# Optimization experiments

Measured on AMD Instinct MI355X. Metric: run time of the kernel, lower is better.

The kernel has to match this reference:

```python
import jax, jax.numpy as jnp
import numpy as np
import math

B, N, DIM, H, D = 2, 2048, 1024, 16, 64
EXPECTED_K = 1.0
LAYERSCALE_INIT = 0.001
EPS = 1e-6  # flax LayerNorm default


def layer_norm(x, scale, bias):
    mu = jnp.mean(x, axis=-1, keepdims=True)
    var = jnp.mean((x - mu) ** 2, axis=-1, keepdims=True)
    return (x - mu) * jax.lax.rsqrt(var + EPS) * scale + bias


def setup_inputs() -> dict:
    key = jax.random.key(0)
    ks = jax.random.split(key, 8)
    s = DIM ** -0.5
    x = jax.random.normal(ks[0], (B, N, DIM), jnp.float32)
    Wq = jax.random.normal(ks[1], (DIM, H * D), jnp.float32) * s
    Wk = jax.random.normal(ks[2], (DIM, H * D), jnp.float32) * s
    Wv = jax.random.normal(ks[3], (DIM, H * D), jnp.float32) * s
    Wo = jax.random.normal(ks[4], (H * D, DIM), jnp.float32) * ((H * D) ** -0.5)
    e = EXPECTED_K / N
    init_bias = jnp.full((1, 1, 1, 1), math.log(e / (1.0 - e)), jnp.float32)
    return {
        'x': x,
        'Wq': Wq, 'bq': jnp.zeros((H * D,), jnp.float32),
        'Wk': Wk, 'bk': jnp.zeros((H * D,), jnp.float32),
        'Wv': Wv, 'bv': jnp.zeros((H * D,), jnp.float32),
        'qn_scale': jnp.ones((D,), jnp.float32), 'qn_bias': jnp.zeros((D,), jnp.float32),
        'kn_scale': jnp.ones((D,), jnp.float32), 'kn_bias': jnp.zeros((D,), jnp.float32),
        'init_bias': init_bias,
        'Wo': Wo, 'bo': jnp.zeros((DIM,), jnp.float32),
        'gamma': jnp.full((DIM,), LAYERSCALE_INIT, jnp.float32),
    }


def reference(x, Wq, bq, Wk, bk, Wv, bv, qn_scale, qn_bias, kn_scale, kn_bias,
              init_bias, Wo, bo, gamma):
    Bv, Nv, _ = x.shape
    q = (x @ Wq + bq).reshape(Bv, Nv, H, D)
    k = (x @ Wk + bk).reshape(Bv, Nv, H, D)
    v = (x @ Wv + bv).reshape(Bv, Nv, H, D)
    q = layer_norm(q, qn_scale, qn_bias)
    k = layer_norm(k, kn_scale, kn_bias)
    q = jnp.swapaxes(q, 1, 2)  # [B,H,N,D]
    k = jnp.swapaxes(k, 1, 2)
    v = jnp.swapaxes(v, 1, 2)
    # NOTE: original code computes scale = head_dim**-0.5 but never applies it.
    attn_logits = jnp.einsum('bhid,bhjd->bhij', q, k)
    attn_weights = jax.nn.sigmoid(attn_logits + init_bias)
    out = jnp.einsum('bhij,bhjd->bhid', attn_weights, v)
    out = jnp.swapaxes(out, 1, 2).reshape(Bv, Nv, H * D)
    out = out @ Wo + bo
    return out * gamma
```

## Files before the change

kernel.cpp:

```cpp
#include <hip/hip_runtime.h>

#define DEV static __device__ __forceinline__

typedef __bf16 bf16x8 __attribute__((ext_vector_type(8)));
typedef __bf16 bf16x4 __attribute__((ext_vector_type(4)));
typedef float f32x4 __attribute__((ext_vector_type(4)));
typedef float f32x16 __attribute__((ext_vector_type(16)));
typedef unsigned int uint4v __attribute__((ext_vector_type(4)));
typedef unsigned short ushort4v __attribute__((ext_vector_type(4)));
using u16 = unsigned short;

#define NN 2048
#define DIMD 1024

DEV u16 f2bf(float f) {
    __bf16 b = (__bf16)f;
    return __builtin_bit_cast(u16, b);
}
DEV float bf2f(u16 s) {
    unsigned u = ((unsigned)s) << 16;
    return __builtin_bit_cast(float, u);
}
DEV bf16x8 load16(const u16* p) { return __builtin_bit_cast(bf16x8, *(const uint4v*)p); }
DEV f32x4 mfma16(bf16x8 a, bf16x8 b, f32x4 c) {
    return __builtin_amdgcn_mfma_f32_16x16x32_bf16(a, b, c, 0, 0, 0);
}
DEV f32x16 mfma32(bf16x8 a, bf16x8 b, f32x16 c) {
    return __builtin_amdgcn_mfma_f32_32x32x16_bf16(a, b, c, 0, 0, 0);
}
DEV void gl_lds16(const u16* g, u16* l) {
    __builtin_amdgcn_global_load_lds((const __attribute__((address_space(1))) void*)g,
                                     (__attribute__((address_space(3))) void*)l, 16, 0, 0);
}


__global__ __launch_bounds__(256) void k_prep(const float* __restrict__ x,
                                              const float* __restrict__ s0,
                                              const float* __restrict__ s1,
                                              const float* __restrict__ s2,
                                              const float* __restrict__ s3,
                                              u16* __restrict__ xb,
                                              u16* __restrict__ wqkv_t,
                                              u16* __restrict__ wo_t) {
    __shared__ float tile[32][33];
    const int z = blockIdx.z;
    if (z < 4) {
        const float* src = (z == 0) ? s0 : (z == 1) ? s1 : (z == 2) ? s2 : s3;
        u16* dst = (z < 3) ? (wqkv_t + (size_t)z * 1024 * 1024) : wo_t;
        int tx = threadIdx.x & 31, ty = threadIdx.x >> 5;
        int kb = blockIdx.y * 32, nb = blockIdx.x * 32;
#pragma unroll
        for (int j = 0; j < 4; ++j)
            tile[ty + 8 * j][tx] = src[(size_t)(kb + ty + 8 * j) * 1024 + nb + tx];
        __syncthreads();
#pragma unroll
        for (int j = 0; j < 4; ++j)
            dst[(size_t)(nb + ty + 8 * j) * 1024 + kb + tx] = f2bf(tile[tx][ty + 8 * j]);
    } else {
        const int bidx = blockIdx.y * 32 + blockIdx.x;
#pragma unroll
        for (int q = 0; q < 4; ++q) {
            int i = bidx * 1024 + q * 256 + threadIdx.x;
            float4 v = ((const float4*)x)[i];
            ushort4v o;
            o[0] = f2bf(v.x); o[1] = f2bf(v.y); o[2] = f2bf(v.z); o[3] = f2bf(v.w);
            *(ushort4v*)(xb + (size_t)i * 4) = o;
        }
    }
}

__global__ __launch_bounds__(256) void k_gemm_qkv(const u16* __restrict__ A,
                                                  const u16* __restrict__ Bt,
                                                  const float* __restrict__ bq,
                                                  const float* __restrict__ bk,
                                                  const float* __restrict__ bv,
                                                  const float* __restrict__ qs,
                                                  const float* __restrict__ qb,
                                                  const float* __restrict__ ks,
                                                  const float* __restrict__ kb_,
                                                  u16* __restrict__ Qf,
                                                  u16* __restrict__ Kf,
                                                  u16* __restrict__ Vf) {
    __shared__ u16 lds[4][2][64 * 32 * 2];
    const int K = 1024;
    const int m0 = blockIdx.x * 128, n0 = blockIdx.y * 128;
    const int tid = threadIdx.x;
    const int lane = tid & 63, w = tid >> 6;
    const int wr = w >> 1, wc = w & 1;
    const int li = lane & 15, g = lane >> 4;
    const int l7 = li & 7;

    f32x4 acc[4][4] = {};

    u16* lA = &lds[w][0][0];
    u16* lB = &lds[w][1][0];
    const int lr = lane >> 3;
    const int lc = (lane & 7) ^ lr;
    const u16* gA = A + (size_t)(m0 + wr * 64 + lr) * K + lc * 8;
    const u16* gB = Bt + (size_t)(n0 + wc * 64 + lr) * K + lc * 8;

    auto STAGE = [&](int k0) {
#pragma unroll
        for (int i = 0; i < 8; ++i) {
            gl_lds16(gA + (size_t)(i * 8) * K + k0, lA + i * 512);
            gl_lds16(gB + (size_t)(i * 8) * K + k0, lB + i * 512);
        }
    };

    STAGE(0);
    asm volatile("s_waitcnt vmcnt(0)" ::: "memory");

    for (int t = 0; t < 16; ++t) {
        bf16x8 af[4][2], bfv[4][2];
#pragma unroll
        for (int mi = 0; mi < 4; ++mi) {
            const int row = mi * 16 + li;
#pragma unroll
            for (int s = 0; s < 2; ++s)
                af[mi][s] = load16(&lA[row * 64 + (((s * 4 + g) ^ l7) * 8)]);
        }
#pragma unroll
        for (int ni = 0; ni < 4; ++ni) {
            const int row = ni * 16 + li;
#pragma unroll
            for (int s = 0; s < 2; ++s)
                bfv[ni][s] = load16(&lB[row * 64 + (((s * 4 + g) ^ l7) * 8)]);
        }
        asm volatile("s_waitcnt lgkmcnt(0)" ::: "memory");
        __builtin_amdgcn_sched_barrier(0);
        if (t < 15) STAGE((t + 1) * 64);
#pragma unroll
        for (int mi = 0; mi < 4; ++mi)
#pragma unroll
            for (int ni = 0; ni < 4; ++ni) {
                acc[mi][ni] = mfma16(af[mi][0], bfv[ni][0], acc[mi][ni]);
                acc[mi][ni] = mfma16(af[mi][1], bfv[ni][1], acc[mi][ni]);
            }
        asm volatile("s_waitcnt vmcnt(0)" ::: "memory");
    }

    const int col0 = n0 + wc * 64;
    const int seg = col0 >> 10;
    const int hcol = col0 & 1023;
    const int h = hcol >> 6;

    if (seg < 2) {
        const float* S = (seg == 0) ? qs : ks;
        const float* Bb = (seg == 0) ? qb : kb_;
        const float* bias = (seg == 0) ? bq : bk;
        u16* dst = (seg == 0) ? Qf : Kf;
        const float sc = (seg == 0) ? -1.44269504f : 1.0f;
        float lnS[4], lnB[4], bv4[4];
#pragma unroll
        for (int ni = 0; ni < 4; ++ni) {
            int d = ni * 16 + li;
            lnS[ni] = S[d] * sc; lnB[ni] = Bb[d] * sc; bv4[ni] = bias[hcol + d];
        }
#pragma unroll
        for (int mi = 0; mi < 4; ++mi) {
#pragma unroll
            for (int r = 0; r < 4; ++r) {
                float v0 = acc[mi][0][r] + bv4[0];
                float v1 = acc[mi][1][r] + bv4[1];
                float v2 = acc[mi][2][r] + bv4[2];
                float v3 = acc[mi][3][r] + bv4[3];
                float s1 = v0 + v1 + v2 + v3;
                float s2 = v0 * v0 + v1 * v1 + v2 * v2 + v3 * v3;
#pragma unroll
                for (int o = 1; o < 16; o <<= 1) {
                    s1 += __shfl_xor(s1, o);
                    s2 += __shfl_xor(s2, o);
                }
                float mu = s1 * (1.0f / 64.0f);
                float var = s2 * (1.0f / 64.0f) - mu * mu;
                float rsv = rsqrtf(var + 1e-6f);
                int row = m0 + wr * 64 + mi * 16 + 4 * g + r;
                int bseq = row >> 11, n = row & 2047;
                size_t base = ((size_t)(bseq * 16 + h)) * 131072 +
                              ((size_t)(n >> 5) * 4) * 512 + (size_t)(n & 31) * 8 +
                              (li >> 3) * 256 + (li & 7);
                dst[base + 0 * 512] = f2bf((v0 - mu) * rsv * lnS[0] + lnB[0]);
                dst[base + 1 * 512] = f2bf((v1 - mu) * rsv * lnS[1] + lnB[1]);
                dst[base + 2 * 512] = f2bf((v2 - mu) * rsv * lnS[2] + lnB[2]);
                dst[base + 3 * 512] = f2bf((v3 - mu) * rsv * lnS[3] + lnB[3]);
            }
        }
    } else {
        float bv4[4];
#pragma unroll
        for (int ni = 0; ni < 4; ++ni) bv4[ni] = bv[hcol + ni * 16 + li];
#pragma unroll
        for (int mi = 0; mi < 4; ++mi) {
#pragma unroll
            for (int r = 0; r < 4; ++r) {
                int row = m0 + wr * 64 + mi * 16 + 4 * g + r;
                int bseq = row >> 11, j = row & 2047;
                size_t vb_ = ((size_t)(bseq * 16 + h)) * 131072 +
                             ((size_t)((j >> 5) * 4 + ((j >> 4) & 1))) * 512 +
                             (size_t)(((j >> 3) & 1) * 32) * 8 + (j & 7);
#pragma unroll
                for (int ni = 0; ni < 4; ++ni)
                    Vf[vb_ + (ni >> 1) * 1024 + ((ni & 1) * 16 + li) * 8] =
                        f2bf(acc[mi][ni][r] + bv4[ni]);
            }
        }
    }
}

__global__ __launch_bounds__(256) void k_gemm_out(const u16* __restrict__ A,
                                                  const u16* __restrict__ Bt,
                                                  const float* __restrict__ bias,
                                                  const float* __restrict__ gamma,
                                                  float* __restrict__ out) {
    __shared__ u16 lds[4][2][64 * 32 * 2];
    const int K = 1024, ldc = 1024;
    const int m0 = blockIdx.x * 128, n0 = blockIdx.y * 128;
    const int tid = threadIdx.x;
    const int lane = tid & 63, w = tid >> 6;
    const int wr = w >> 1, wc = w & 1;
    const int li = lane & 15, g = lane >> 4;
    const int l7 = li & 7;

    f32x4 acc[4][4] = {};

    u16* lA = &lds[w][0][0];
    u16* lB = &lds[w][1][0];
    const int lr = lane >> 3;
    const int lc = (lane & 7) ^ lr;
    const u16* gA = A + (size_t)(m0 + wr * 64 + lr) * K + lc * 8;
    const u16* gB = Bt + (size_t)(n0 + wc * 64 + lr) * K + lc * 8;

    auto STAGE = [&](int k0) {
#pragma unroll
        for (int i = 0; i < 8; ++i) {
            gl_lds16(gA + (size_t)(i * 8) * K + k0, lA + i * 512);
            gl_lds16(gB + (size_t)(i * 8) * K + k0, lB + i * 512);
        }
    };

    STAGE(0);
    asm volatile("s_waitcnt vmcnt(0)" ::: "memory");

    for (int t = 0; t < 16; ++t) {
        bf16x8 af[4][2], bfv[4][2];
#pragma unroll
        for (int mi = 0; mi < 4; ++mi) {
            const int row = mi * 16 + li;
#pragma unroll
            for (int s = 0; s < 2; ++s)
                af[mi][s] = load16(&lA[row * 64 + (((s * 4 + g) ^ l7) * 8)]);
        }
#pragma unroll
        for (int ni = 0; ni < 4; ++ni) {
            const int row = ni * 16 + li;
#pragma unroll
            for (int s = 0; s < 2; ++s)
                bfv[ni][s] = load16(&lB[row * 64 + (((s * 4 + g) ^ l7) * 8)]);
        }
        asm volatile("s_waitcnt lgkmcnt(0)" ::: "memory");
        __builtin_amdgcn_sched_barrier(0);
        if (t < 15) STAGE((t + 1) * 64);
#pragma unroll
        for (int mi = 0; mi < 4; ++mi)
#pragma unroll
            for (int ni = 0; ni < 4; ++ni) {
                acc[mi][ni] = mfma16(af[mi][0], bfv[ni][0], acc[mi][ni]);
                acc[mi][ni] = mfma16(af[mi][1], bfv[ni][1], acc[mi][ni]);
            }
        asm volatile("s_waitcnt vmcnt(0)" ::: "memory");
    }

#pragma unroll
    for (int mi = 0; mi < 4; ++mi) {
        int row = m0 + wr * 64 + mi * 16 + 4 * g;
#pragma unroll
        for (int ni = 0; ni < 4; ++ni) {
            int col = n0 + wc * 64 + ni * 16 + li;
            float bv_ = bias[col], gv = gamma[col];
            f32x4 v = acc[mi][ni];
#pragma unroll
            for (int r = 0; r < 4; ++r)
                out[(size_t)(row + r) * ldc + col] = (v[r] + bv_) * gv;
        }
    }
}

__global__ __launch_bounds__(256, 2) void k_attn(const u16* __restrict__ Qf,
                                                 const u16* __restrict__ Kf,
                                                 const u16* __restrict__ Vf,
                                                 const float* __restrict__ ib,
                                                 u16* __restrict__ attn_out) {
    __shared__ float red[2][64][65];
    const int bid = blockIdx.x;
    const int xcd = bid & 7, idx = bid >> 3;
    const int bh = xcd * 4 + (idx >> 5);
    const int iblk = idx & 31;
    const int b = bh >> 4, h = bh & 15;
    const int tid = threadIdx.x;
    const int jq = tid >> 6, lane = tid & 63;
    const int l32 = lane & 31, hi = lane >> 5;
    const float c0 = -ib[0] * 1.44269504f;
    const u16* Qb = Qf + (size_t)bh * 131072;
    const u16* Kb = Kf + (size_t)bh * 131072;
    const u16* Vb = Vf + (size_t)bh * 131072;
    const int it0 = iblk * 2;

    bf16x8 qf[2][4];
#pragma unroll
    for (int t = 0; t < 2; ++t)
#pragma unroll
        for (int s = 0; s < 4; ++s)
            qf[t][s] = load16(Qb + ((size_t)((it0 + t) * 4 + s)) * 512 + lane * 8);

    f32x16 accO[2][2] = {};
    const u16* kb0 = Kb + (size_t)(jq * 16) * 2048;
    const u16* vb0 = Vb + (size_t)(jq * 16) * 2048;

    f32x16 cinit;
#pragma unroll
    for (int r = 0; r < 16; ++r) cinit[r] = c0;

    bf16x8 kf[2][4], vf[2][2][2];
#pragma unroll
    for (int s = 0; s < 4; ++s) kf[0][s] = load16(kb0 + s * 512 + lane * 8);
#pragma unroll
    for (int s = 0; s < 4; ++s) kf[1][s] = load16(kb0 + 2048 + s * 512 + lane * 8);
#pragma unroll
    for (int db = 0; db < 2; ++db)
#pragma unroll
        for (int js = 0; js < 2; ++js)
            vf[0][db][js] = load16(vb0 + (db * 2 + js) * 512 + lane * 8);
    f32x16 sa0 = cinit, sa1;
#pragma unroll
    for (int s = 0; s < 4; ++s) sa0 = mfma32(kf[0][s], qf[0][s], sa0);

#pragma unroll 2
    for (int jt = 0; jt < 16; ++jt) {
        const int cur = jt & 1, nxt = cur ^ 1;
        if (jt < 15) {
            const u16* vbn = vb0 + (size_t)(jt + 1) * 2048;
#pragma unroll
            for (int db = 0; db < 2; ++db)
#pragma unroll
                for (int js = 0; js < 2; ++js)
                    vf[nxt][db][js] = load16(vbn + (db * 2 + js) * 512 + lane * 8);
        }
        __builtin_amdgcn_s_setprio(1);
        sa1 = cinit;
#pragma unroll
        for (int s = 0; s < 4; ++s) sa1 = mfma32(kf[cur][s], qf[1][s], sa1);
        __builtin_amdgcn_s_setprio(0);
        if (jt < 14) {
            const u16* kbn = kb0 + (size_t)(jt + 2) * 2048;
#pragma unroll
            for (int s = 0; s < 4; ++s) kf[cur][s] = load16(kbn + s * 512 + lane * 8);
        }
        bf16x8 p00, p01;
        {
            float p[16];
#pragma unroll
            for (int r = 0; r < 16; ++r) {
                float e = __builtin_amdgcn_exp2f(sa0[r]);
                p[r] = __builtin_amdgcn_rcpf(1.0f + e);
            }
            unsigned wd[8];
#pragma unroll
            for (int u2 = 0; u2 < 8; ++u2) {
                unsigned r_;
                asm("v_cvt_pk_bf16_f32 %0, %1, %2"
                    : "=v"(r_) : "v"(p[2 * u2]), "v"(p[2 * u2 + 1]));
                wd[u2] = r_;
            }
            asm("v_permlane32_swap_b32 %0, %1" : "+v"(wd[0]), "+v"(wd[2]));
            asm("v_permlane32_swap_b32 %0, %1" : "+v"(wd[1]), "+v"(wd[3]));
            asm("v_permlane32_swap_b32 %0, %1" : "+v"(wd[4]), "+v"(wd[6]));
            asm("v_permlane32_swap_b32 %0, %1" : "+v"(wd[5]), "+v"(wd[7]));
            uint4v u0 = {wd[0], wd[1], wd[2], wd[3]};
            uint4v u1 = {wd[4], wd[5], wd[6], wd[7]};
            p00 = __builtin_bit_cast(bf16x8, u0);
            p01 = __builtin_bit_cast(bf16x8, u1);
        }
        __builtin_amdgcn_s_setprio(1);
        accO[0][0] = mfma32(vf[cur][0][0], p00, accO[0][0]);
        accO[0][0] = mfma32(vf[cur][0][1], p01, accO[0][0]);
        accO[0][1] = mfma32(vf[cur][1][0], p00, accO[0][1]);
        accO[0][1] = mfma32(vf[cur][1][1], p01, accO[0][1]);
        if (jt < 15) {
            sa0 = cinit;
#pragma unroll
            for (int s = 0; s < 4; ++s) sa0 = mfma32(kf[nxt][s], qf[0][s], sa0);
        }
        __builtin_amdgcn_s_setprio(0);
        bf16x8 p10, p11;
        {
            float p[16];
#pragma unroll
            for (int r = 0; r < 16; ++r) {
                float e = __builtin_amdgcn_exp2f(sa1[r]);
                p[r] = __builtin_amdgcn_rcpf(1.0f + e);
            }
            unsigned wd[8];
#pragma unroll
            for (int u2 = 0; u2 < 8; ++u2) {
                unsigned r_;
                asm("v_cvt_pk_bf16_f32 %0, %1, %2"
                    : "=v"(r_) : "v"(p[2 * u2]), "v"(p[2 * u2 + 1]));
                wd[u2] = r_;
            }
            asm("v_permlane32_swap_b32 %0, %1" : "+v"(wd[0]), "+v"(wd[2]));
            asm("v_permlane32_swap_b32 %0, %1" : "+v"(wd[1]), "+v"(wd[3]));
            asm("v_permlane32_swap_b32 %0, %1" : "+v"(wd[4]), "+v"(wd[6]));
            asm("v_permlane32_swap_b32 %0, %1" : "+v"(wd[5]), "+v"(wd[7]));
            uint4v u0 = {wd[0], wd[1], wd[2], wd[3]};
            uint4v u1 = {wd[4], wd[5], wd[6], wd[7]};
            p10 = __builtin_bit_cast(bf16x8, u0);
            p11 = __builtin_bit_cast(bf16x8, u1);
        }
        __builtin_amdgcn_s_setprio(1);
        accO[1][0] = mfma32(vf[cur][0][0], p10, accO[1][0]);
        accO[1][0] = mfma32(vf[cur][0][1], p11, accO[1][0]);
        accO[1][1] = mfma32(vf[cur][1][0], p10, accO[1][1]);
        accO[1][1] = mfma32(vf[cur][1][1], p11, accO[1][1]);
        __builtin_amdgcn_s_setprio(0);
    }

    if (jq & 1) {
#pragma unroll
        for (int t = 0; t < 2; ++t)
#pragma unroll
            for (int db = 0; db < 2; ++db)
#pragma unroll
                for (int r = 0; r < 16; ++r)
                    red[jq >> 1][t * 32 + l32][db * 32 + (r & 3) + 8 * (r >> 2) + 4 * hi] =
                        accO[t][db][r];
    }
    __syncthreads();
    if (!(jq & 1)) {
#pragma unroll
        for (int t = 0; t < 2; ++t)
#pragma unroll
            for (int db = 0; db < 2; ++db)
#pragma unroll
                for (int r = 0; r < 16; ++r)
                    accO[t][db][r] +=
                        red[jq >> 1][t * 32 + l32][db * 32 + (r & 3) + 8 * (r >> 2) + 4 * hi];
    }
    __syncthreads();
    if (jq == 2) {
#pragma unroll
        for (int t = 0; t < 2; ++t)
#pragma unroll
            for (int db = 0; db < 2; ++db)
#pragma unroll
                for (int r = 0; r < 16; ++r)
                    red[0][t * 32 + l32][db * 32 + (r & 3) + 8 * (r >> 2) + 4 * hi] =
                        accO[t][db][r];
    }
    __syncthreads();
    if (jq == 0) {
#pragma unroll
        for (int t = 0; t < 2; ++t)
#pragma unroll
            for (int db = 0; db < 2; ++db)
#pragma unroll
                for (int r = 0; r < 16; ++r)
                    accO[t][db][r] +=
                        red[0][t * 32 + l32][db * 32 + (r & 3) + 8 * (r >> 2) + 4 * hi];
#pragma unroll
        for (int t = 0; t < 2; ++t) {
            const int i = it0 * 32 + t * 32 + l32;
#pragma unroll
            for (int db = 0; db < 2; ++db)
#pragma unroll
                for (int q = 0; q < 4; ++q) {
                    int d = db * 32 + 8 * q + 4 * hi;
                    bf16x4 o4;
#pragma unroll
                    for (int r = 0; r < 4; ++r) o4[r] = (__bf16)accO[t][db][4 * q + r];
                    *(bf16x4*)&attn_out[(size_t)(b * NN + i) * 1024 + h * 64 + d] = o4;
                }
        }
    }
}


extern "C" void kernel_launch(void* const* d_in, const int* in_sizes, int n_in,
                              void* d_out, int out_size, void* d_ws, size_t ws_size,
                              hipStream_t stream) {
    (void)in_sizes; (void)n_in; (void)out_size; (void)ws_size;
    const float* x     = (const float*)d_in[0];
    const float* Wq    = (const float*)d_in[1];
    const float* bq    = (const float*)d_in[2];
    const float* Wk    = (const float*)d_in[3];
    const float* bk    = (const float*)d_in[4];
    const float* Wv    = (const float*)d_in[5];
    const float* bv    = (const float*)d_in[6];
    const float* qn_s  = (const float*)d_in[7];
    const float* qn_b  = (const float*)d_in[8];
    const float* kn_s  = (const float*)d_in[9];
    const float* kn_b  = (const float*)d_in[10];
    const float* ib    = (const float*)d_in[11];
    const float* Wo    = (const float*)d_in[12];
    const float* bo    = (const float*)d_in[13];
    const float* gamma = (const float*)d_in[14];
    float* out = (float*)d_out;

    char* ws = (char*)d_ws;
    size_t off = 0;
    auto alloc = [&](size_t bytes) -> void* {
        void* p = ws + off;
        off += (bytes + 255) & ~(size_t)255;
        return p;
    };
    u16* xb       = (u16*)alloc((size_t)4096 * 1024 * 2);
    u16* wqkv_t   = (u16*)alloc((size_t)3072 * 1024 * 2);
    u16* wo_t     = (u16*)alloc((size_t)1024 * 1024 * 2);
    u16* Qf       = (u16*)alloc((size_t)32 * 131072 * 2);
    u16* Kf       = (u16*)alloc((size_t)32 * 131072 * 2);
    u16* Vf       = (u16*)alloc((size_t)32 * 131072 * 2);
    u16* attn_out = (u16*)alloc((size_t)4096 * 1024 * 2);

    k_prep<<<dim3(32, 32, 5), 256, 0, stream>>>(x, Wq, Wk, Wv, Wo, xb, wqkv_t, wo_t);
    k_gemm_qkv<<<dim3(32, 24), 256, 0, stream>>>(xb, wqkv_t, bq, bk, bv,
                                                 qn_s, qn_b, kn_s, kn_b, Qf, Kf, Vf);
    k_attn<<<1024, 256, 0, stream>>>(Qf, Kf, Vf, ib, attn_out);
    k_gemm_out<<<dim3(32, 8), 256, 0, stream>>>(attn_out, wo_t, bo, gamma, out);
}
```

Before: 116.5 us.

## Use 256x256 shared-LDS tiles with double-buffered prefetch in QKV GEMM

Rewrites the QKV projection GEMM to use 512-thread blocks computing 256x256 output tiles. Operand tiles now sit in LDS shared by all eight waves instead of each wave keeping its own private copy. Loads are double-buffered two k-steps ahead and MFMA blocks run at raised priority via setprio. The goal is fewer global reads per FLOP and load latency hidden behind compute. The cost is only 192 blocks on a 256-CU part, more registers for the 8x4 accumulators, and extra block-wide barriers.

```diff
diff --git a/kernel.cpp b/kernel.cpp
--- a/kernel.cpp
+++ b/kernel.cpp
@@ -69,66 +69,72 @@
     }
 }
 
-__global__ __launch_bounds__(256) void k_gemm_qkv(const u16* __restrict__ A,
-                                                  const u16* __restrict__ Bt,
-                                                  const float* __restrict__ bq,
-                                                  const float* __restrict__ bk,
-                                                  const float* __restrict__ bv,
-                                                  const float* __restrict__ qs,
-                                                  const float* __restrict__ qb,
-                                                  const float* __restrict__ ks,
-                                                  const float* __restrict__ kb_,
-                                                  u16* __restrict__ Qf,
-                                                  u16* __restrict__ Kf,
-                                                  u16* __restrict__ Vf) {
-    __shared__ u16 lds[4][2][64 * 32 * 2];
+__global__ __launch_bounds__(512, 2) void k_gemm_qkv(const u16* __restrict__ A,
+                                                     const u16* __restrict__ Bt,
+                                                     const float* __restrict__ bq,
+                                                     const float* __restrict__ bk,
+                                                     const float* __restrict__ bv,
+                                                     const float* __restrict__ qs,
+                                                     const float* __restrict__ qb,
+                                                     const float* __restrict__ ks,
+                                                     const float* __restrict__ kb_,
+                                                     u16* __restrict__ Qf,
+                                                     u16* __restrict__ Kf,
+                                                     u16* __restrict__ Vf) {
+    __shared__ u16 As[2][256 * 64];
+    __shared__ u16 Bs[2][256 * 64];
     const int K = 1024;
-    const int m0 = blockIdx.x * 128, n0 = blockIdx.y * 128;
+    const int m0 = blockIdx.x * 256, n0 = blockIdx.y * 256;
     const int tid = threadIdx.x;
     const int lane = tid & 63, w = tid >> 6;
-    const int wr = w >> 1, wc = w & 1;
+    const int wm = w >> 2, wn = w & 3;
     const int li = lane & 15, g = lane >> 4;
     const int l7 = li & 7;
 
-    f32x4 acc[4][4] = {};
-
-    u16* lA = &lds[w][0][0];
-    u16* lB = &lds[w][1][0];
+    f32x4 acc[8][4] = {};
+
     const int lr = lane >> 3;
     const int lc = (lane & 7) ^ lr;
-    const u16* gA = A + (size_t)(m0 + wr * 64 + lr) * K + lc * 8;
-    const u16* gB = Bt + (size_t)(n0 + wc * 64 + lr) * K + lc * 8;
-
-    auto STAGE = [&](int k0) {
-#pragma unroll
-        for (int i = 0; i < 8; ++i) {
+    const u16* gA = A + (size_t)(m0 + w * 32 + lr) * K + lc * 8;
+    const u16* gB = Bt + (size_t)(n0 + w * 32 + lr) * K + lc * 8;
+
+    auto STAGE = [&](int buf, int k0) {
+        u16* lA = &As[buf][w * 2048];
+        u16* lB = &Bs[buf][w * 2048];
+#pragma unroll
+        for (int i = 0; i < 4; ++i) {
             gl_lds16(gA + (size_t)(i * 8) * K + k0, lA + i * 512);
             gl_lds16(gB + (size_t)(i * 8) * K + k0, lB + i * 512);
         }
     };
 
-    STAGE(0);
-    asm volatile("s_waitcnt vmcnt(0)" ::: "memory");
+    STAGE(0, 0);
+    STAGE(1, 64);
+    asm volatile("s_waitcnt vmcnt(8)" ::: "memory");
+    __syncthreads();
 
     for (int t = 0; t < 16; ++t) {
-        bf16x8 af[4][2], bfv[4][2];
+        const int cur = t & 1;
+        const u16* as = As[cur];
+        const u16* bs = Bs[cur];
+        bf16x8 bfv[4][2], af[4][2];
+#pragma unroll
+        for (int ni = 0; ni < 4; ++ni) {
+            const int row = wn * 64 + ni * 16 + li;
+#pragma unroll
+            for (int s = 0; s < 2; ++s)
+                bfv[ni][s] = load16(&bs[row * 64 + (((s * 4 + g) ^ l7) * 8)]);
+        }
 #pragma unroll
         for (int mi = 0; mi < 4; ++mi) {
-            const int row = mi * 16 + li;
+            const int row = wm * 128 + mi * 16 + li;
 #pragma unroll
             for (int s = 0; s < 2; ++s)
-                af[mi][s] = load16(&lA[row * 64 + (((s * 4 + g) ^ l7) * 8)]);
-        }
-#pragma unroll
-        for (int ni = 0; ni < 4; ++ni) {
-            const int row = ni * 16 + li;
-#pragma unroll
-            for (int s = 0; s < 2; ++s)
-                bfv[ni][s] = load16(&lB[row * 64 + (((s * 4 + g) ^ l7) * 8)]);
+                af[mi][s] = load16(&as[row * 64 + (((s * 4 + g) ^ l7) * 8)]);
         }
         asm volatile("s_waitcnt lgkmcnt(0)" ::: "memory");
         __builtin_amdgcn_sched_barrier(0);
-        if (t < 15) STAGE((t + 1) * 64);
+        __builtin_amdgcn_s_setprio(1);
 #pragma unroll
         for (int mi = 0; mi < 4; ++mi)
 #pragma unroll
@@ -136,10 +142,37 @@
                 acc[mi][ni] = mfma16(af[mi][0], bfv[ni][0], acc[mi][ni]);
                 acc[mi][ni] = mfma16(af[mi][1], bfv[ni][1], acc[mi][ni]);
             }
-        asm volatile("s_waitcnt vmcnt(0)" ::: "memory");
-    }
-
-    const int col0 = n0 + wc * 64;
+        __builtin_amdgcn_s_setprio(0);
+#pragma unroll
+        for (int mi = 0; mi < 4; ++mi) {
+            const int row = wm * 128 + 64 + mi * 16 + li;
+#pragma unroll
+            for (int s = 0; s < 2; ++s)
+                af[mi][s] = load16(&as[row * 64 + (((s * 4 + g) ^ l7) * 8)]);
+        }
+        asm volatile("s_waitcnt lgkmcnt(0)" ::: "memory");
+        __builtin_amdgcn_sched_barrier(0);
+        __builtin_amdgcn_s_setprio(1);
+#pragma unroll
+        for (int mi = 0; mi < 4; ++mi)
+#pragma unroll
+            for (int ni = 0; ni < 4; ++ni) {
+                acc[mi + 4][ni] = mfma16(af[mi][0], bfv[ni][0], acc[mi + 4][ni]);
+                acc[mi + 4][ni] = mfma16(af[mi][1], bfv[ni][1], acc[mi + 4][ni]);
+            }
+        __builtin_amdgcn_s_setprio(0);
+        __syncthreads();
+        if (t < 14) STAGE(cur, (t + 2) * 64);
+        if (t < 15) {
+            if (t < 14)
+                asm volatile("s_waitcnt vmcnt(8)" ::: "memory");
+            else
+                asm volatile("s_waitcnt vmcnt(0)" ::: "memory");
+            __syncthreads();
+        }
+    }
+
+    const int col0 = n0 + wn * 64;
     const int seg = col0 >> 10;
     const int hcol = col0 & 1023;
     const int h = hcol >> 6;
@@ -157,7 +190,7 @@
             lnS[ni] = S[d] * sc; lnB[ni] = Bb[d] * sc; bv4[ni] = bias[hcol + d];
         }
 #pragma unroll
-        for (int mi = 0; mi < 4; ++mi) {
+        for (int mi = 0; mi < 8; ++mi) {
 #pragma unroll
             for (int r = 0; r < 4; ++r) {
                 float v0 = acc[mi][0][r] + bv4[0];
@@ -174,7 +207,7 @@
                 float mu = s1 * (1.0f / 64.0f);
                 float var = s2 * (1.0f / 64.0f) - mu * mu;
                 float rsv = rsqrtf(var + 1e-6f);
-                int row = m0 + wr * 64 + mi * 16 + 4 * g + r;
+                int row = m0 + wm * 128 + mi * 16 + 4 * g + r;
                 int bseq = row >> 11, n = row & 2047;
                 size_t base = ((size_t)(bseq * 16 + h)) * 131072 +
                               ((size_t)(n >> 5) * 4) * 512 + (size_t)(n & 31) * 8 +
@@ -190,10 +223,10 @@
 #pragma unroll
         for (int ni = 0; ni < 4; ++ni) bv4[ni] = bv[hcol + ni * 16 + li];
 #pragma unroll
-        for (int mi = 0; mi < 4; ++mi) {
+        for (int mi = 0; mi < 8; ++mi) {
 #pragma unroll
             for (int r = 0; r < 4; ++r) {
-                int row = m0 + wr * 64 + mi * 16 + 4 * g + r;
+                int row = m0 + wm * 128 + mi * 16 + 4 * g + r;
                 int bseq = row >> 11, j = row & 2047;
                 size_t vb_ = ((size_t)(bseq * 16 + h)) * 131072 +
                              ((size_t)((j >> 5) * 4 + ((j >> 4) & 1))) * 512 +
@@ -521,7 +554,7 @@
     u16* attn_out = (u16*)alloc((size_t)4096 * 1024 * 2);
 
     k_prep<<<dim3(32, 32, 5), 256, 0, stream>>>(x, Wq, Wk, Wv, Wo, xb, wqkv_t, wo_t);
-    k_gemm_qkv<<<dim3(32, 24), 256, 0, stream>>>(xb, wqkv_t, bq, bk, bv,
+    k_gemm_qkv<<<dim3(16, 12), 512, 0, stream>>>(xb, wqkv_t, bq, bk, bv,
                                                  qn_s, qn_b, kn_s, kn_b, Qf, Kf, Vf);
     k_attn<<<1024, 256, 0, stream>>>(Qf, Kf, Vf, ib, attn_out);
     k_gemm_out<<<dim3(32, 8), 256, 0, stream>>>(attn_out, wo_t, bo, gamma, out);
```

Result: slower. 119.4 us (+2.5%).
